# Performance work log

Measured on AMD Instinct MI355X. Metric: run time of the kernel, lower is better.

Reference implementation:

```python
import jax, jax.numpy as jnp
import numpy as np

H = 8        # num_heads
D = 768      # d_model
DH = D // H  # d_head = 96


def setup_inputs() -> dict:
    key = jax.random.key(0)
    ks = jax.random.split(key, 12)
    B, S = 4, 2048
    s_in = 1.0 / np.sqrt(D)
    s_cat = 1.0 / np.sqrt(D)
    return {
        "input_querys": jax.random.normal(ks[0], (B, S, D), jnp.float32),
        "input_key": jax.random.normal(ks[1], (B, S, D), jnp.float32),
        "input_values": jax.random.normal(ks[2], (B, S, D), jnp.float32),
        # per-head projection weights, stacked over the head axis
        "Wq": jax.random.normal(ks[3], (H, D, DH), jnp.float32) * s_in,
        "bq": jax.random.normal(ks[4], (H, DH), jnp.float32) * s_in,
        "Wk": jax.random.normal(ks[5], (H, D, DH), jnp.float32) * s_in,
        "bk": jax.random.normal(ks[6], (H, DH), jnp.float32) * s_in,
        "Wv": jax.random.normal(ks[7], (H, D, DH), jnp.float32) * s_in,
        "bv": jax.random.normal(ks[8], (H, DH), jnp.float32) * s_in,
        # output linear: (H*DH) -> D
        "Wo": jax.random.normal(ks[9], (H * DH, D), jnp.float32) * s_cat,
        "bo": jax.random.normal(ks[10], (D,), jnp.float32) * s_cat,
    }


def reference(input_querys, input_key, input_values, Wq, bq, Wk, bk, Wv, bv, Wo, bo):
    # Per-head linear projections (vectorized over the head axis)
    # q/k/v: [B,S,D] -> [B,H,S,DH]
    Q = jnp.einsum("bsd,hdk->bhsk", input_querys, Wq) + bq[None, :, None, :]
    K = jnp.einsum("bsd,hdk->bhsk", input_key, Wk) + bk[None, :, None, :]
    V = jnp.einsum("bsd,hdk->bhsk", input_values, Wv) + bv[None, :, None, :]

    scale = 1.0 / jnp.sqrt(jnp.asarray(DH, Q.dtype))
    scores = jnp.einsum("bhsk,bhtk->bhst", Q, K) * scale  # [B,H,S,S]
    attn = jax.nn.softmax(scores, axis=-1)
    out = jnp.einsum("bhst,bhtk->bhsk", attn, V)  # [B,H,S,DH]

    # concat heads (head-major order matches torch.cat over ModuleList)
    B, _, S, _ = out.shape
    cat = out.transpose(0, 2, 1, 3).reshape(B, S, H * DH)
    return cat @ Wo + bo
```

## Files before the change

kernel.cpp:

```cpp
#include <hip/hip_runtime.h>


typedef unsigned short u16;
typedef _Float16 h16;
typedef h16 h16x8 __attribute__((ext_vector_type(8)));
typedef __fp16 fp16x2 __attribute__((ext_vector_type(2)));
typedef unsigned short u16x8 __attribute__((ext_vector_type(8)));
typedef unsigned short u16x4 __attribute__((ext_vector_type(4)));
typedef float f32x4 __attribute__((ext_vector_type(4)));

__device__ __forceinline__ u16 f2h(float f) {
  union { h16 h; u16 u; } c; c.h = (h16)f; return c.u;
}

__device__ __forceinline__ void gll16(const void* g, void* l) {
  __builtin_amdgcn_global_load_lds(
      (const __attribute__((address_space(1))) void*)g,
      (__attribute__((address_space(3))) void*)l, 16, 0, 0);
}

__global__ __launch_bounds__(256) void prep_kernel(
    const float* __restrict__ Wq, const float* __restrict__ Wk,
    const float* __restrict__ Wv, const float* __restrict__ Wo,
    const float* __restrict__ Xk, const float* __restrict__ Xv,
    u16* __restrict__ WqT, u16* __restrict__ WkT,
    u16* __restrict__ WvT, u16* __restrict__ WoT,
    u16* __restrict__ Xk16, u16* __restrict__ Xv16)
{
  const long gid = (long)blockIdx.x * 256 + threadIdx.x;
  if (gid >= 294912) {
    long i = gid - 294912;
    const int t = (i >= 786432) ? 1 : 0;
    const long e = (i - (long)t * 786432) * 8;
    const float* src = t ? Xv : Xk;
    u16* dst = t ? Xv16 : Xk16;
    f32x4 a = *(const f32x4*)(&src[e]);
    f32x4 b = *(const f32x4*)(&src[e + 4]);
    u16x8 v;
    #pragma unroll
    for (int j = 0; j < 4; j++) { v[j] = f2h(a[j]); v[4 + j] = f2h(b[j]); }
    *(u16x8*)(&dst[e]) = v;
    return;
  }
  int idx = (int)gid * 8;
  int region = idx / 589824;
  int i = idx % 589824;
  int n = i / 768;
  int d = i % 768;
  u16x8 v;
  if (region == 3) {
    #pragma unroll
    for (int j = 0; j < 8; j++) v[j] = f2h(Wo[(size_t)(d + j) * 768 + n]);
    *(u16x8*)(&WoT[i]) = v;
  } else {
    int h = n / 96, kk = n % 96;
    const float* W = (region == 0) ? Wq : (region == 1) ? Wk : Wv;
    u16* T = (region == 0) ? WqT : (region == 1) ? WkT : WvT;
    #pragma unroll
    for (int j = 0; j < 8; j++) v[j] = f2h(W[(size_t)h * 73728 + (size_t)(d + j) * 96 + kk]);
    *(u16x8*)(&T[i]) = v;
  }
}

#define GK 768

__global__ __launch_bounds__(256) void gemm_qkv(
    const float* __restrict__ Xq, const u16* __restrict__ Xk16,
    const u16* __restrict__ Xv16, const u16* __restrict__ WT,
    const float* __restrict__ bq, const float* __restrict__ bk,
    const float* __restrict__ bv,
    u16* __restrict__ Q16, u16* __restrict__ K16, u16* __restrict__ VT)
{
  const int z = blockIdx.z;
  const u16* BT = WT + (size_t)z * 589824;
  const float* bias = (z == 0) ? bq : (z == 1) ? bk : bv;

  __shared__ __align__(16) u16 As[128 * 32];
  __shared__ __align__(16) u16 Bs[64 * 32];
  const int tid = threadIdx.x;
  const int wave = tid >> 6;
  const int lane = tid & 63;
  const int quad = lane >> 4;
  const int l16 = lane & 15;
  const int m0 = blockIdx.x * 128;
  const int n0 = blockIdx.y * 64;

  f32x4 acc[2][4];
  #pragma unroll
  for (int i = 0; i < 2; i++)
    #pragma unroll
    for (int j = 0; j < 4; j++) acc[i][j] = (f32x4){0.f, 0.f, 0.f, 0.f};

  if (z == 0) {
    const float* A = Xq;
    const int ar = tid >> 2;
    const int ac = (tid & 3) * 8;

    f32x4 pf[4];
    u16x8 pb;
    {
      pf[0] = *(const f32x4*)(&A[(size_t)(m0 + ar) * GK + ac]);
      pf[1] = *(const f32x4*)(&A[(size_t)(m0 + ar) * GK + ac + 4]);
      pf[2] = *(const f32x4*)(&A[(size_t)(m0 + 64 + ar) * GK + ac]);
      pf[3] = *(const f32x4*)(&A[(size_t)(m0 + 64 + ar) * GK + ac + 4]);
      pb = *(const u16x8*)(&BT[(size_t)(n0 + ar) * GK + ac]);
    }

    for (int kt = 0; kt < 24; kt++) {
      u16x8 h0, h1;
      #pragma unroll
      for (int j = 0; j < 4; j++) {
        h0[j] = f2h(pf[0][j]); h0[4 + j] = f2h(pf[1][j]);
        h1[j] = f2h(pf[2][j]); h1[4 + j] = f2h(pf[3][j]);
      }
      *(u16x8*)(&As[ar * 32 + ac]) = h0;
      *(u16x8*)(&As[(64 + ar) * 32 + ac]) = h1;
      *(u16x8*)(&Bs[ar * 32 + ac]) = pb;
      __syncthreads();

      if (kt + 1 < 24) {
        const int k0 = (kt + 1) * 32;
        pf[0] = *(const f32x4*)(&A[(size_t)(m0 + ar) * GK + k0 + ac]);
        pf[1] = *(const f32x4*)(&A[(size_t)(m0 + ar) * GK + k0 + ac + 4]);
        pf[2] = *(const f32x4*)(&A[(size_t)(m0 + 64 + ar) * GK + k0 + ac]);
        pf[3] = *(const f32x4*)(&A[(size_t)(m0 + 64 + ar) * GK + k0 + ac + 4]);
        pb = *(const u16x8*)(&BT[(size_t)(n0 + ar) * GK + k0 + ac]);
      }

      h16x8 af[2], bf[4];
      #pragma unroll
      for (int mf = 0; mf < 2; mf++)
        af[mf] = *(const h16x8*)(&As[(wave * 32 + mf * 16 + l16) * 32 + quad * 8]);
      #pragma unroll
      for (int nf = 0; nf < 4; nf++)
        bf[nf] = *(const h16x8*)(&Bs[(nf * 16 + l16) * 32 + quad * 8]);
      #pragma unroll
      for (int mf = 0; mf < 2; mf++)
        #pragma unroll
        for (int nf = 0; nf < 4; nf++)
          acc[mf][nf] = __builtin_amdgcn_mfma_f32_16x16x32_f16(af[mf], bf[nf], acc[mf][nf], 0, 0, 0);

      if (kt + 1 < 24) __syncthreads();
    }
  } else {
    const u16* A = (z == 1) ? Xk16 : Xv16;
    const int Lr = lane >> 2, Lc = (lane & 3) * 8;
    const u16* gA0 = A + (size_t)(m0 + wave * 32 + Lr) * GK + Lc;
    const u16* gA1 = gA0 + (size_t)16 * GK;
    const u16* gB  = BT + (size_t)(n0 + wave * 16 + Lr) * GK + Lc;
    u16* lA0 = &As[(wave * 32) * 32];
    u16* lA1 = &As[(wave * 32 + 16) * 32];
    u16* lB  = &Bs[(wave * 16) * 32];

    for (int kt = 0; kt < 24; kt++) {
      gll16(gA0, lA0);
      gll16(gA1, lA1);
      gll16(gB, lB);
      gA0 += 32; gA1 += 32; gB += 32;
      __syncthreads();

      h16x8 af[2], bf[4];
      #pragma unroll
      for (int mf = 0; mf < 2; mf++)
        af[mf] = *(const h16x8*)(&As[(wave * 32 + mf * 16 + l16) * 32 + quad * 8]);
      #pragma unroll
      for (int nf = 0; nf < 4; nf++)
        bf[nf] = *(const h16x8*)(&Bs[(nf * 16 + l16) * 32 + quad * 8]);
      #pragma unroll
      for (int mf = 0; mf < 2; mf++)
        #pragma unroll
        for (int nf = 0; nf < 4; nf++)
          acc[mf][nf] = __builtin_amdgcn_mfma_f32_16x16x32_f16(af[mf], bf[nf], acc[mf][nf], 0, 0, 0);
      __syncthreads();
    }
  }

  u16* Yr = (z == 0) ? Q16 : K16;
  #pragma unroll
  for (int nf = 0; nf < 4; nf++) {
    const int n = n0 + nf * 16 + l16;
    const float bv2 = bias[n];
    #pragma unroll
    for (int mf = 0; mf < 2; mf++) {
      const int m = m0 + wave * 32 + mf * 16 + quad * 4;
      if (z == 2) {
        const int b = m >> 11, s = m & 2047;
        u16x4 pk;
        #pragma unroll
        for (int r = 0; r < 4; r++) pk[r] = f2h(acc[mf][nf][r] + bv2);
        *(u16x4*)(&VT[(size_t)b * 768 * 2048 + (size_t)n * 2048 + s]) = pk;
      } else {
        #pragma unroll
        for (int r = 0; r < 4; r++)
          Yr[(size_t)(m + r) * GK + n] = f2h(acc[mf][nf][r] + bv2);
      }
    }
  }
}

__global__ __launch_bounds__(256) void gemm_o(
    const u16* __restrict__ A, const u16* __restrict__ BT,
    const float* __restrict__ bias, float* __restrict__ Y)
{
  __shared__ __align__(16) u16 As[128 * 32];
  __shared__ __align__(16) u16 Bs[64 * 32];
  const int tid = threadIdx.x;
  const int wave = tid >> 6;
  const int lane = tid & 63;
  const int quad = lane >> 4;
  const int l16 = lane & 15;
  const int m0 = blockIdx.x * 128;
  const int n0 = blockIdx.y * 64;

  f32x4 acc[2][4];
  #pragma unroll
  for (int i = 0; i < 2; i++)
    #pragma unroll
    for (int j = 0; j < 4; j++) acc[i][j] = (f32x4){0.f, 0.f, 0.f, 0.f};

  const int Lr = lane >> 2, Lc = (lane & 3) * 8;
  const u16* gA0 = A + (size_t)(m0 + wave * 32 + Lr) * GK + Lc;
  const u16* gA1 = gA0 + (size_t)16 * GK;
  const u16* gB  = BT + (size_t)(n0 + wave * 16 + Lr) * GK + Lc;
  u16* lA0 = &As[(wave * 32) * 32];
  u16* lA1 = &As[(wave * 32 + 16) * 32];
  u16* lB  = &Bs[(wave * 16) * 32];

  for (int kt = 0; kt < 24; kt++) {
    gll16(gA0, lA0);
    gll16(gA1, lA1);
    gll16(gB, lB);
    gA0 += 32; gA1 += 32; gB += 32;
    __syncthreads();

    h16x8 af[2], bf[4];
    #pragma unroll
    for (int mf = 0; mf < 2; mf++)
      af[mf] = *(const h16x8*)(&As[(wave * 32 + mf * 16 + l16) * 32 + quad * 8]);
    #pragma unroll
    for (int nf = 0; nf < 4; nf++)
      bf[nf] = *(const h16x8*)(&Bs[(nf * 16 + l16) * 32 + quad * 8]);
    #pragma unroll
    for (int mf = 0; mf < 2; mf++)
      #pragma unroll
      for (int nf = 0; nf < 4; nf++)
        acc[mf][nf] = __builtin_amdgcn_mfma_f32_16x16x32_f16(af[mf], bf[nf], acc[mf][nf], 0, 0, 0);
    __syncthreads();
  }

  #pragma unroll
  for (int nf = 0; nf < 4; nf++) {
    const int n = n0 + nf * 16 + l16;
    const float bv = bias[n];
    #pragma unroll
    for (int mf = 0; mf < 2; mf++) {
      const int m = m0 + wave * 32 + mf * 16 + quad * 4;
      #pragma unroll
      for (int r = 0; r < 4; r++)
        Y[(size_t)(m + r) * GK + n] = acc[mf][nf][r] + bv;
    }
  }
}

#define SEQ 2048
#define LQK 104
#define LVT 72
#define LPS 72

__global__ __launch_bounds__(512, 4) void attn_kernel(
    const u16* __restrict__ Q, const u16* __restrict__ K,
    const u16* __restrict__ VT, u16* __restrict__ O)
{
  __shared__ __align__(16) u16 Ks[64 * LQK];
  __shared__ __align__(16) u16 Vt[96 * LVT];
  __shared__ __align__(16) u16 Ps[8][16 * LPS];

  const int tid = threadIdx.x;
  const int wave = tid >> 6;
  const int lane = tid & 63;
  const int quad = lane >> 4;
  const int l16 = lane & 15;

  const int bh = blockIdx.y;
  const int b = bh >> 3, h = bh & 7;
  const int q0 = blockIdx.x * 128;

  const size_t batch_off = (size_t)b * SEQ * 768;
  const u16* Kg = K + batch_off + h * 96;
  const u16* Vg = VT + (size_t)b * 768 * 2048 + (size_t)(h * 96) * 2048;

  h16x8 qf[3];
  {
    const u16* Qrow = Q + batch_off + (size_t)(q0 + wave * 16 + l16) * 768 + h * 96 + quad * 8;
    #pragma unroll
    for (int ks = 0; ks < 3; ks++) qf[ks] = *(const h16x8*)(&Qrow[ks * 32]);
  }

  const int kr0 = tid / 12, kc0 = (tid % 12) * 8;
  const int kr1 = (tid + 512) / 12, kc1 = ((tid + 512) % 12) * 8;
  const int vr0 = tid >> 3, vc0 = (tid & 7) * 8;
  const int vr1 = (tid + 512) >> 3, vc1 = ((tid + 512) & 7) * 8;
  const bool extra = tid < 256;

  f32x4 o[6];
  #pragma unroll
  for (int i = 0; i < 6; i++) o[i] = (f32x4){0.f, 0.f, 0.f, 0.f};
  float m_raw = -1e30f, lrow = 0.f;
  const float sc = 0.14724498f;

  u16* Pw = &Ps[wave][0];

  u16x8 kA, kB, vA, vB;
  kA = *(const u16x8*)(&Kg[(size_t)kr0 * 768 + kc0]);
  vA = *(const u16x8*)(&Vg[(size_t)vr0 * 2048 + vc0]);
  if (extra) {
    kB = *(const u16x8*)(&Kg[(size_t)kr1 * 768 + kc1]);
    vB = *(const u16x8*)(&Vg[(size_t)vr1 * 2048 + vc1]);
  }

  for (int kt = 0; kt < SEQ / 64; kt++) {
    *(u16x8*)(&Ks[kr0 * LQK + kc0]) = kA;
    *(u16x8*)(&Vt[vr0 * LVT + vc0]) = vA;
    if (extra) {
      *(u16x8*)(&Ks[kr1 * LQK + kc1]) = kB;
      *(u16x8*)(&Vt[vr1 * LVT + vc1]) = vB;
    }
    __syncthreads();

    if (kt + 1 < SEQ / 64) {
      const u16* Kn = Kg + (size_t)(kt + 1) * 64 * 768;
      const u16* Vn = Vg + (size_t)(kt + 1) * 64;
      kA = *(const u16x8*)(&Kn[(size_t)kr0 * 768 + kc0]);
      vA = *(const u16x8*)(&Vn[(size_t)vr0 * 2048 + vc0]);
      if (extra) {
        kB = *(const u16x8*)(&Kn[(size_t)kr1 * 768 + kc1]);
        vB = *(const u16x8*)(&Vn[(size_t)vr1 * 2048 + vc1]);
      }
    }

    f32x4 s[4];
    #pragma unroll
    for (int kf = 0; kf < 4; kf++) s[kf] = (f32x4){0.f, 0.f, 0.f, 0.f};
    __builtin_amdgcn_s_setprio(1);
    #pragma unroll
    for (int ks = 0; ks < 3; ks++) {
      #pragma unroll
      for (int kf = 0; kf < 4; kf++) {
        h16x8 a = *(const h16x8*)(&Ks[(kf * 16 + l16) * LQK + ks * 32 + quad * 8]);
        s[kf] = __builtin_amdgcn_mfma_f32_16x16x32_f16(a, qf[ks], s[kf], 0, 0, 0);
      }
    }
    __builtin_amdgcn_s_setprio(0);

    float mx = s[0][0];
    #pragma unroll
    for (int kf = 0; kf < 4; kf++)
      #pragma unroll
      for (int r = 0; r < 4; r++) mx = fmaxf(mx, s[kf][r]);
    mx = fmaxf(mx, __shfl_xor(mx, 16));
    mx = fmaxf(mx, __shfl_xor(mx, 32));
    if (__any(mx > m_raw + 54.0f)) {
      const float mnew = fmaxf(m_raw, mx);
      const float alpha = exp2f(sc * (m_raw - mnew));
      lrow *= alpha;
      #pragma unroll
      for (int nfo = 0; nfo < 6; nfo++)
        #pragma unroll
        for (int r = 0; r < 4; r++) o[nfo][r] *= alpha;
      m_raw = mnew;
    }
    const float c0 = sc * m_raw;
    float ps = 0.f;
    #pragma unroll
    for (int kf = 0; kf < 4; kf++)
      #pragma unroll
      for (int r = 0; r < 4; r++) {
        float p = exp2f(fmaf(s[kf][r], sc, -c0));
        s[kf][r] = p;
        ps += p;
      }
    lrow += ps;

    #pragma unroll
    for (int kf = 0; kf < 4; kf++)
      #pragma unroll
      for (int rp = 0; rp < 4; rp += 2) {
        fp16x2 pk = __builtin_amdgcn_cvt_pkrtz(s[kf][rp], s[kf][rp + 1]);
        *(fp16x2*)(&Pw[l16 * LPS + kf * 16 + quad * 4 + rp]) = pk;
      }

    __builtin_amdgcn_s_setprio(1);
    #pragma unroll
    for (int ks = 0; ks < 2; ks++) {
      h16x8 pfr = *(const h16x8*)(&Pw[l16 * LPS + ks * 32 + quad * 8]);
      #pragma unroll
      for (int nfo = 0; nfo < 6; nfo++) {
        h16x8 vfr = *(const h16x8*)(&Vt[(nfo * 16 + l16) * LVT + ks * 32 + quad * 8]);
        o[nfo] = __builtin_amdgcn_mfma_f32_16x16x32_f16(vfr, pfr, o[nfo], 0, 0, 0);
      }
    }
    __builtin_amdgcn_s_setprio(0);
    __syncthreads();
  }

  lrow += __shfl_xor(lrow, 16);
  lrow += __shfl_xor(lrow, 32);
  const float inv = 1.0f / lrow;
  u16* Ob = O + batch_off + (size_t)(q0 + wave * 16 + l16) * 768 + h * 96;
  #pragma unroll
  for (int nfo = 0; nfo < 6; nfo++) {
    fp16x2 lo = __builtin_amdgcn_cvt_pkrtz(o[nfo][0] * inv, o[nfo][1] * inv);
    fp16x2 hi = __builtin_amdgcn_cvt_pkrtz(o[nfo][2] * inv, o[nfo][3] * inv);
    *(fp16x2*)(&Ob[nfo * 16 + quad * 4]) = lo;
    *(fp16x2*)(&Ob[nfo * 16 + quad * 4 + 2]) = hi;
  }
}

extern "C" void kernel_launch(void* const* d_in, const int* in_sizes, int n_in,
                              void* d_out, int out_size, void* d_ws, size_t ws_size,
                              hipStream_t stream) {
  const float* Xq = (const float*)d_in[0];
  const float* Xk = (const float*)d_in[1];
  const float* Xv = (const float*)d_in[2];
  const float* Wq = (const float*)d_in[3];
  const float* bq = (const float*)d_in[4];
  const float* Wk = (const float*)d_in[5];
  const float* bk = (const float*)d_in[6];
  const float* Wv = (const float*)d_in[7];
  const float* bv = (const float*)d_in[8];
  const float* Wo = (const float*)d_in[9];
  const float* bo = (const float*)d_in[10];

  u16* wsu = (u16*)d_ws;
  u16* WT   = wsu;
  u16* WoT  = wsu + 3 * 589824;
  u16* Q16  = wsu + 4 * 589824;
  u16* Xk16 = Q16 + 6291456;
  u16* Xv16 = Xk16 + 6291456;

  u16* outu = (u16*)d_out;
  u16* VTb = outu;
  u16* K16 = outu + 6291456;

  u16* A16 = (u16*)d_in[0];

  prep_kernel<<<7296, 256, 0, stream>>>(Wq, Wk, Wv, Wo, Xk, Xv,
                                        WT, WT + 589824, WT + 2 * 589824, WoT,
                                        Xk16, Xv16);
  gemm_qkv<<<dim3(64, 12, 3), 256, 0, stream>>>(Xq, Xk16, Xv16, WT, bq, bk, bv, Q16, K16, VTb);
  attn_kernel<<<dim3(16, 32), 512, 0, stream>>>(Q16, K16, VTb, A16);
  gemm_o<<<dim3(64, 12), 256, 0, stream>>>(A16, WoT, bo, (float*)d_out);
}
```

Measured before the change: 299.9 us.

## Process two query tiles per wave in attention and pre-convert Xq to fp16

The attention kernel goes from 8 waves handling 16 query rows each to 4 waves handling 32 rows each. Each K/V fragment read from shared memory now feeds two MFMAs, which halves LDS traffic per FLOP and needs fewer threads to stage the K/V tiles. In exchange it roughly doubles accumulator and score registers per wave and removes the explicit occupancy hint. Separately, when the workspace is large enough, the prep kernel also converts Xq to fp16, so the Q projection uses the same direct global-to-LDS load path as K and V instead of converting fp32 inside the GEMM loop.

```diff
diff --git a/kernel.cpp b/kernel.cpp
--- a/kernel.cpp
+++ b/kernel.cpp
@@ -23,17 +23,18 @@
     const float* __restrict__ Wq, const float* __restrict__ Wk,
     const float* __restrict__ Wv, const float* __restrict__ Wo,
     const float* __restrict__ Xk, const float* __restrict__ Xv,
+    const float* __restrict__ Xq,
     u16* __restrict__ WqT, u16* __restrict__ WkT,
     u16* __restrict__ WvT, u16* __restrict__ WoT,
-    u16* __restrict__ Xk16, u16* __restrict__ Xv16)
+    u16* __restrict__ Xk16, u16* __restrict__ Xv16, u16* __restrict__ Xq16)
 {
   const long gid = (long)blockIdx.x * 256 + threadIdx.x;
   if (gid >= 294912) {
     long i = gid - 294912;
-    const int t = (i >= 786432) ? 1 : 0;
-    const long e = (i - (long)t * 786432) * 8;
-    const float* src = t ? Xv : Xk;
-    u16* dst = t ? Xv16 : Xk16;
+    const int t = (int)(i / 786432);
+    const long e = (i % 786432) * 8;
+    const float* src = (t == 0) ? Xk : (t == 1) ? Xv : Xq;
+    u16* dst = (t == 0) ? Xk16 : (t == 1) ? Xv16 : Xq16;
     f32x4 a = *(const f32x4*)(&src[e]);
     f32x4 b = *(const f32x4*)(&src[e + 4]);
     u16x8 v;
@@ -65,11 +66,13 @@
 #define GK 768
 
 __global__ __launch_bounds__(256) void gemm_qkv(
-    const float* __restrict__ Xq, const u16* __restrict__ Xk16,
-    const u16* __restrict__ Xv16, const u16* __restrict__ WT,
+    const float* __restrict__ XqF, const u16* __restrict__ Xq16,
+    const u16* __restrict__ Xk16, const u16* __restrict__ Xv16,
+    const u16* __restrict__ WT,
     const float* __restrict__ bq, const float* __restrict__ bk,
     const float* __restrict__ bv,
-    u16* __restrict__ Q16, u16* __restrict__ K16, u16* __restrict__ VT)
+    u16* __restrict__ Q16, u16* __restrict__ K16, u16* __restrict__ VT,
+    int qfp32)
 {
   const int z = blockIdx.z;
   const u16* BT = WT + (size_t)z * 589824;
@@ -91,8 +94,8 @@
     #pragma unroll
     for (int j = 0; j < 4; j++) acc[i][j] = (f32x4){0.f, 0.f, 0.f, 0.f};
 
-  if (z == 0) {
-    const float* A = Xq;
+  if (z == 0 && qfp32) {
+    const float* A = XqF;
     const int ar = tid >> 2;
     const int ac = (tid & 3) * 8;
 
@@ -143,7 +146,7 @@
       if (kt + 1 < 24) __syncthreads();
     }
   } else {
-    const u16* A = (z == 1) ? Xk16 : Xv16;
+    const u16* A = (z == 0) ? Xq16 : (z == 1) ? Xk16 : Xv16;
     const int Lr = lane >> 2, Lc = (lane & 3) * 8;
     const u16* gA0 = A + (size_t)(m0 + wave * 32 + Lr) * GK + Lc;
     const u16* gA1 = gA0 + (size_t)16 * GK;
@@ -267,13 +270,13 @@
 #define LVT 72
 #define LPS 72
 
-__global__ __launch_bounds__(512, 4) void attn_kernel(
+__global__ __launch_bounds__(256) void attn_kernel(
     const u16* __restrict__ Q, const u16* __restrict__ K,
     const u16* __restrict__ VT, u16* __restrict__ O)
 {
   __shared__ __align__(16) u16 Ks[64 * LQK];
   __shared__ __align__(16) u16 Vt[96 * LVT];
-  __shared__ __align__(16) u16 Ps[8][16 * LPS];
+  __shared__ __align__(16) u16 Ps[4][32 * LPS];
 
   const int tid = threadIdx.x;
   const int wave = tid >> 6;
@@ -289,130 +292,147 @@
   const u16* Kg = K + batch_off + h * 96;
   const u16* Vg = VT + (size_t)b * 768 * 2048 + (size_t)(h * 96) * 2048;
 
-  h16x8 qf[3];
-  {
-    const u16* Qrow = Q + batch_off + (size_t)(q0 + wave * 16 + l16) * 768 + h * 96 + quad * 8;
-    #pragma unroll
-    for (int ks = 0; ks < 3; ks++) qf[ks] = *(const h16x8*)(&Qrow[ks * 32]);
-  }
-
-  const int kr0 = tid / 12, kc0 = (tid % 12) * 8;
-  const int kr1 = (tid + 512) / 12, kc1 = ((tid + 512) % 12) * 8;
-  const int vr0 = tid >> 3, vc0 = (tid & 7) * 8;
-  const int vr1 = (tid + 512) >> 3, vc1 = ((tid + 512) & 7) * 8;
-  const bool extra = tid < 256;
-
-  f32x4 o[6];
-  #pragma unroll
-  for (int i = 0; i < 6; i++) o[i] = (f32x4){0.f, 0.f, 0.f, 0.f};
-  float m_raw = -1e30f, lrow = 0.f;
+  h16x8 qf[2][3];
+  #pragma unroll
+  for (int mf = 0; mf < 2; mf++) {
+    const u16* Qrow = Q + batch_off +
+        (size_t)(q0 + wave * 32 + mf * 16 + l16) * 768 + h * 96 + quad * 8;
+    #pragma unroll
+    for (int ks = 0; ks < 3; ks++) qf[mf][ks] = *(const h16x8*)(&Qrow[ks * 32]);
+  }
+
+  int krr[3], kcc[3], vrr[3], vcc[3];
+  #pragma unroll
+  for (int j = 0; j < 3; j++) {
+    const int ik = tid + j * 256;
+    krr[j] = ik / 12; kcc[j] = (ik % 12) * 8;
+    vrr[j] = ik >> 3; vcc[j] = (ik & 7) * 8;
+  }
+
+  f32x4 o[2][6];
+  #pragma unroll
+  for (int mf = 0; mf < 2; mf++)
+    #pragma unroll
+    for (int i = 0; i < 6; i++) o[mf][i] = (f32x4){0.f, 0.f, 0.f, 0.f};
+  float m_raw[2] = {-1e30f, -1e30f};
+  float lrow[2] = {0.f, 0.f};
   const float sc = 0.14724498f;
 
   u16* Pw = &Ps[wave][0];
 
-  u16x8 kA, kB, vA, vB;
-  kA = *(const u16x8*)(&Kg[(size_t)kr0 * 768 + kc0]);
-  vA = *(const u16x8*)(&Vg[(size_t)vr0 * 2048 + vc0]);
-  if (extra) {
-    kB = *(const u16x8*)(&Kg[(size_t)kr1 * 768 + kc1]);
-    vB = *(const u16x8*)(&Vg[(size_t)vr1 * 2048 + vc1]);
+  u16x8 kA[3], vA[3];
+  #pragma unroll
+  for (int j = 0; j < 3; j++) {
+    kA[j] = *(const u16x8*)(&Kg[(size_t)krr[j] * 768 + kcc[j]]);
+    vA[j] = *(const u16x8*)(&Vg[(size_t)vrr[j] * 2048 + vcc[j]]);
   }
 
   for (int kt = 0; kt < SEQ / 64; kt++) {
-    *(u16x8*)(&Ks[kr0 * LQK + kc0]) = kA;
-    *(u16x8*)(&Vt[vr0 * LVT + vc0]) = vA;
-    if (extra) {
-      *(u16x8*)(&Ks[kr1 * LQK + kc1]) = kB;
-      *(u16x8*)(&Vt[vr1 * LVT + vc1]) = vB;
+    #pragma unroll
+    for (int j = 0; j < 3; j++) {
+      *(u16x8*)(&Ks[krr[j] * LQK + kcc[j]]) = kA[j];
+      *(u16x8*)(&Vt[vrr[j] * LVT + vcc[j]]) = vA[j];
     }
     __syncthreads();
 
     if (kt + 1 < SEQ / 64) {
       const u16* Kn = Kg + (size_t)(kt + 1) * 64 * 768;
       const u16* Vn = Vg + (size_t)(kt + 1) * 64;
-      kA = *(const u16x8*)(&Kn[(size_t)kr0 * 768 + kc0]);
-      vA = *(const u16x8*)(&Vn[(size_t)vr0 * 2048 + vc0]);
-      if (extra) {
-        kB = *(const u16x8*)(&Kn[(size_t)kr1 * 768 + kc1]);
-        vB = *(const u16x8*)(&Vn[(size_t)vr1 * 2048 + vc1]);
-      }
-    }
-
-    f32x4 s[4];
-    #pragma unroll
-    for (int kf = 0; kf < 4; kf++) s[kf] = (f32x4){0.f, 0.f, 0.f, 0.f};
+      #pragma unroll
+      for (int j = 0; j < 3; j++) {
+        kA[j] = *(const u16x8*)(&Kn[(size_t)krr[j] * 768 + kcc[j]]);
+        vA[j] = *(const u16x8*)(&Vn[(size_t)vrr[j] * 2048 + vcc[j]]);
+      }
+    }
+
+    f32x4 s[2][4];
+    #pragma unroll
+    for (int mf = 0; mf < 2; mf++)
+      #pragma unroll
+      for (int kf = 0; kf < 4; kf++) s[mf][kf] = (f32x4){0.f, 0.f, 0.f, 0.f};
     __builtin_amdgcn_s_setprio(1);
     #pragma unroll
     for (int ks = 0; ks < 3; ks++) {
       #pragma unroll
       for (int kf = 0; kf < 4; kf++) {
         h16x8 a = *(const h16x8*)(&Ks[(kf * 16 + l16) * LQK + ks * 32 + quad * 8]);
-        s[kf] = __builtin_amdgcn_mfma_f32_16x16x32_f16(a, qf[ks], s[kf], 0, 0, 0);
+        s[0][kf] = __builtin_amdgcn_mfma_f32_16x16x32_f16(a, qf[0][ks], s[0][kf], 0, 0, 0);
+        s[1][kf] = __builtin_amdgcn_mfma_f32_16x16x32_f16(a, qf[1][ks], s[1][kf], 0, 0, 0);
       }
     }
     __builtin_amdgcn_s_setprio(0);
 
-    float mx = s[0][0];
-    #pragma unroll
-    for (int kf = 0; kf < 4; kf++)
-      #pragma unroll
-      for (int r = 0; r < 4; r++) mx = fmaxf(mx, s[kf][r]);
-    mx = fmaxf(mx, __shfl_xor(mx, 16));
-    mx = fmaxf(mx, __shfl_xor(mx, 32));
-    if (__any(mx > m_raw + 54.0f)) {
-      const float mnew = fmaxf(m_raw, mx);
-      const float alpha = exp2f(sc * (m_raw - mnew));
-      lrow *= alpha;
-      #pragma unroll
-      for (int nfo = 0; nfo < 6; nfo++)
-        #pragma unroll
-        for (int r = 0; r < 4; r++) o[nfo][r] *= alpha;
-      m_raw = mnew;
-    }
-    const float c0 = sc * m_raw;
-    float ps = 0.f;
-    #pragma unroll
-    for (int kf = 0; kf < 4; kf++)
-      #pragma unroll
-      for (int r = 0; r < 4; r++) {
-        float p = exp2f(fmaf(s[kf][r], sc, -c0));
-        s[kf][r] = p;
-        ps += p;
-      }
-    lrow += ps;
-
-    #pragma unroll
-    for (int kf = 0; kf < 4; kf++)
-      #pragma unroll
-      for (int rp = 0; rp < 4; rp += 2) {
-        fp16x2 pk = __builtin_amdgcn_cvt_pkrtz(s[kf][rp], s[kf][rp + 1]);
-        *(fp16x2*)(&Pw[l16 * LPS + kf * 16 + quad * 4 + rp]) = pk;
-      }
+    #pragma unroll
+    for (int mf = 0; mf < 2; mf++) {
+      float mx = s[mf][0][0];
+      #pragma unroll
+      for (int kf = 0; kf < 4; kf++)
+        #pragma unroll
+        for (int r = 0; r < 4; r++) mx = fmaxf(mx, s[mf][kf][r]);
+      mx = fmaxf(mx, __shfl_xor(mx, 16));
+      mx = fmaxf(mx, __shfl_xor(mx, 32));
+      if (__any(mx > m_raw[mf] + 54.0f)) {
+        const float mnew = fmaxf(m_raw[mf], mx);
+        const float alpha = exp2f(sc * (m_raw[mf] - mnew));
+        lrow[mf] *= alpha;
+        #pragma unroll
+        for (int nfo = 0; nfo < 6; nfo++)
+          #pragma unroll
+          for (int r = 0; r < 4; r++) o[mf][nfo][r] *= alpha;
+        m_raw[mf] = mnew;
+      }
+      const float c0 = sc * m_raw[mf];
+      float ps = 0.f;
+      #pragma unroll
+      for (int kf = 0; kf < 4; kf++)
+        #pragma unroll
+        for (int r = 0; r < 4; r++) {
+          float p = exp2f(fmaf(s[mf][kf][r], sc, -c0));
+          s[mf][kf][r] = p;
+          ps += p;
+        }
+      lrow[mf] += ps;
+
+      #pragma unroll
+      for (int kf = 0; kf < 4; kf++)
+        #pragma unroll
+        for (int rp = 0; rp < 4; rp += 2) {
+          fp16x2 pk = __builtin_amdgcn_cvt_pkrtz(s[mf][kf][rp], s[mf][kf][rp + 1]);
+          *(fp16x2*)(&Pw[(mf * 16 + l16) * LPS + kf * 16 + quad * 4 + rp]) = pk;
+        }
+    }
 
     __builtin_amdgcn_s_setprio(1);
     #pragma unroll
     for (int ks = 0; ks < 2; ks++) {
-      h16x8 pfr = *(const h16x8*)(&Pw[l16 * LPS + ks * 32 + quad * 8]);
+      h16x8 pf0 = *(const h16x8*)(&Pw[l16 * LPS + ks * 32 + quad * 8]);
+      h16x8 pf1 = *(const h16x8*)(&Pw[(16 + l16) * LPS + ks * 32 + quad * 8]);
       #pragma unroll
       for (int nfo = 0; nfo < 6; nfo++) {
         h16x8 vfr = *(const h16x8*)(&Vt[(nfo * 16 + l16) * LVT + ks * 32 + quad * 8]);
-        o[nfo] = __builtin_amdgcn_mfma_f32_16x16x32_f16(vfr, pfr, o[nfo], 0, 0, 0);
+        o[0][nfo] = __builtin_amdgcn_mfma_f32_16x16x32_f16(vfr, pf0, o[0][nfo], 0, 0, 0);
+        o[1][nfo] = __builtin_amdgcn_mfma_f32_16x16x32_f16(vfr, pf1, o[1][nfo], 0, 0, 0);
       }
     }
     __builtin_amdgcn_s_setprio(0);
     __syncthreads();
   }
 
-  lrow += __shfl_xor(lrow, 16);
-  lrow += __shfl_xor(lrow, 32);
-  const float inv = 1.0f / lrow;
-  u16* Ob = O + batch_off + (size_t)(q0 + wave * 16 + l16) * 768 + h * 96;
-  #pragma unroll
-  for (int nfo = 0; nfo < 6; nfo++) {
-    fp16x2 lo = __builtin_amdgcn_cvt_pkrtz(o[nfo][0] * inv, o[nfo][1] * inv);
-    fp16x2 hi = __builtin_amdgcn_cvt_pkrtz(o[nfo][2] * inv, o[nfo][3] * inv);
-    *(fp16x2*)(&Ob[nfo * 16 + quad * 4]) = lo;
-    *(fp16x2*)(&Ob[nfo * 16 + quad * 4 + 2]) = hi;
+  #pragma unroll
+  for (int mf = 0; mf < 2; mf++) {
+    float l = lrow[mf];
+    l += __shfl_xor(l, 16);
+    l += __shfl_xor(l, 32);
+    const float inv = 1.0f / l;
+    u16* Ob = O + batch_off +
+        (size_t)(q0 + wave * 32 + mf * 16 + l16) * 768 + h * 96;
+    #pragma unroll
+    for (int nfo = 0; nfo < 6; nfo++) {
+      fp16x2 lo = __builtin_amdgcn_cvt_pkrtz(o[mf][nfo][0] * inv, o[mf][nfo][1] * inv);
+      fp16x2 hi = __builtin_amdgcn_cvt_pkrtz(o[mf][nfo][2] * inv, o[mf][nfo][3] * inv);
+      *(fp16x2*)(&Ob[nfo * 16 + quad * 4]) = lo;
+      *(fp16x2*)(&Ob[nfo * 16 + quad * 4 + 2]) = hi;
+    }
   }
 }
 
@@ -437,6 +457,11 @@
   u16* Q16  = wsu + 4 * 589824;
   u16* Xk16 = Q16 + 6291456;
   u16* Xv16 = Xk16 + 6291456;
+  u16* Xq16 = Xv16 + 6291456;
+
+  const size_t need = (size_t)(4 * 589824 + 4 * 6291456) * 2;
+  const int q16 = (ws_size >= need) ? 1 : 0;
+  const int nx = q16 ? 3 : 2;
 
   u16* outu = (u16*)d_out;
   u16* VTb = outu;
@@ -444,10 +469,11 @@
 
   u16* A16 = (u16*)d_in[0];
 
-  prep_kernel<<<7296, 256, 0, stream>>>(Wq, Wk, Wv, Wo, Xk, Xv,
-                                        WT, WT + 589824, WT + 2 * 589824, WoT,
-                                        Xk16, Xv16);
-  gemm_qkv<<<dim3(64, 12, 3), 256, 0, stream>>>(Xq, Xk16, Xv16, WT, bq, bk, bv, Q16, K16, VTb);
-  attn_kernel<<<dim3(16, 32), 512, 0, stream>>>(Q16, K16, VTb, A16);
+  prep_kernel<<<1152 + 3072 * nx, 256, 0, stream>>>(
+      Wq, Wk, Wv, Wo, Xk, Xv, Xq,
+      WT, WT + 589824, WT + 2 * 589824, WoT, Xk16, Xv16, Xq16);
+  gemm_qkv<<<dim3(64, 12, 3), 256, 0, stream>>>(
+      Xq, Xq16, Xk16, Xv16, WT, bq, bk, bv, Q16, K16, VTb, q16 ? 0 : 1);
+  attn_kernel<<<dim3(16, 32), 256, 0, stream>>>(Q16, K16, VTb, A16);
   gemm_o<<<dim3(64, 12), 256, 0, stream>>>(A16, WoT, bo, (float*)d_out);
 }
```

After: 301.1 us. Within noise of the previous version (+0.4%).
